# Performance work log

Hardware: AMD Instinct MI355X
Metric: run time of the kernel (lower is better)

The kernel has to match this reference:

```python
import jax, jax.numpy as jnp
import numpy as np

N_QUBITS = 6
N_QPARAMS = 15  # 6*5/2 RBS gates in the pyramid circuit


def _pyramid_top_wires(n):
    """Top wire q of each RBS gate (acting on wires (q, q+1)) in pyramid order.
    Diamond/pyramid layer t has gates at q = |n-2-t|, |n-2-t|+2, ... <= n-2;
    total n(n-1)/2 gates (15 for n=6)."""
    qs = []
    for t in range(2 * n - 3):
        for q in range(abs(n - 2 - t), n - 1, 2):
            qs.append(q)
    return qs


def setup_inputs() -> dict:
    key = jax.random.key(0)
    k0, k1, k2, k3 = jax.random.split(key, 4)
    B, H, W = 16384, 64, 64
    D = H * W  # flattened feature dim
    x = jax.random.normal(k0, (B, H, W, 1), dtype=jnp.float32)
    W1 = jax.random.normal(k1, (D, N_QUBITS), dtype=jnp.float32) / np.float32(np.sqrt(D))
    b1 = jnp.zeros((N_QUBITS,), dtype=jnp.float32)
    # quantum_weights: zeros in the original init; use small randn so grads are non-trivial
    qw = 0.1 * jax.random.normal(k2, (N_QPARAMS,), dtype=jnp.float32)
    W2 = jax.random.normal(k3, (N_QUBITS, 1), dtype=jnp.float32) / np.float32(np.sqrt(N_QUBITS))
    b2 = jnp.zeros((1,), dtype=jnp.float32)
    return {"x": x, "W1": W1, "b1": b1, "qw": qw, "W2": W2, "b2": b2}


def reference(x, W1, b1, qw, W2, b2):
    B = x.shape[0]
    xf = x.reshape(B, -1)                       # Flatten
    h = xf @ W1 + b1                            # Dense(6, linear) -> [B, 6]
    # vector_loader(convert_array(h)): amplitude-encode normalized h in the unary basis
    a = h / jnp.linalg.norm(h, axis=1, keepdims=True)   # [B, 6] unary amplitudes
    # pyramid_circuit: 15 RBS gates == Givens rotations on the 6-dim unary subspace
    for k, q in enumerate(_pyramid_top_wires(N_QUBITS)):
        c, s = jnp.cos(qw[k]), jnp.sin(qw[k])
        aq = c * a[:, q] + s * a[:, q + 1]
        aq1 = -s * a[:, q] + c * a[:, q + 1]
        a = a.at[:, q].set(aq).at[:, q + 1].set(aq1)
    # <Z_i> on unary state sum_i a_i |e_i>  ==  1 - 2 a_i^2
    z = 1.0 - 2.0 * a * a                       # [B, 6]
    z = jnp.where(jnp.isnan(z), jnp.zeros_like(z), z)  # NaN guard from original
    return jax.nn.sigmoid(z @ W2 + b2)          # Dense(1, sigmoid) -> [B, 1]
```

## Files before the change

kernel.cpp:

```cpp
#include <hip/hip_runtime.h>
#include <math.h>

#define DFEAT 4096
#define NQ 6
#define ROWS_PER_WAVE 4
#define WAVES_PER_BLOCK 4
#define ROWS_PER_BLOCK (ROWS_PER_WAVE * WAVES_PER_BLOCK)

__global__ __launch_bounds__(256, 4)
void hybrid_fused_kernel(const float* __restrict__ x,
                         const float* __restrict__ W1,
                         const float* __restrict__ b1,
                         const float* __restrict__ qw,
                         const float* __restrict__ W2,
                         const float* __restrict__ b2,
                         float* __restrict__ out, int B)
{
    const int lane = threadIdx.x & 63;
    const int wave_in_block = threadIdx.x >> 6;
    const int row0 = (blockIdx.x * WAVES_PER_BLOCK + wave_in_block) * ROWS_PER_WAVE;
    if (row0 >= B) return;

    const float* xp[ROWS_PER_WAVE];
#pragma unroll
    for (int r = 0; r < ROWS_PER_WAVE; ++r) {
        int rr = row0 + r; if (rr > B - 1) rr = B - 1;
        xp[r] = x + (size_t)rr * DFEAT;
    }

    float acc[ROWS_PER_WAVE][NQ];
#pragma unroll
    for (int r = 0; r < ROWS_PER_WAVE; ++r)
#pragma unroll
        for (int j = 0; j < NQ; ++j) acc[r][j] = 0.0f;

    for (int it = 0; it < DFEAT / 256; ++it) {
        const int d = it * 256 + lane * 4;

        float w[24];
        const float4* wp = reinterpret_cast<const float4*>(W1 + (size_t)d * NQ);
#pragma unroll
        for (int m = 0; m < 6; ++m)
            reinterpret_cast<float4*>(w)[m] = wp[m];

#pragma unroll
        for (int r = 0; r < ROWS_PER_WAVE; ++r) {
            const float4 xv = *reinterpret_cast<const float4*>(xp[r] + d);
            const float xs[4] = {xv.x, xv.y, xv.z, xv.w};
#pragma unroll
            for (int k = 0; k < 4; ++k)
#pragma unroll
                for (int j = 0; j < NQ; ++j)
                    acc[r][j] = fmaf(xs[k], w[k * NQ + j], acc[r][j]);
        }
    }

#pragma unroll
    for (int r = 0; r < ROWS_PER_WAVE; ++r)
#pragma unroll
        for (int j = 0; j < NQ; ++j) {
            float v = acc[r][j];
#pragma unroll
            for (int off = 32; off >= 1; off >>= 1)
                v += __shfl_xor(v, off, 64);
            acc[r][j] = v;
        }

    if (lane < ROWS_PER_WAVE) {
        float h[NQ];
#pragma unroll
        for (int j = 0; j < NQ; ++j) {
            float v = acc[0][j];
            v = (lane == 1) ? acc[1][j] : v;
            v = (lane == 2) ? acc[2][j] : v;
            v = (lane == 3) ? acc[3][j] : v;
            h[j] = v + b1[j];
        }
        float n2 = 0.0f;
#pragma unroll
        for (int j = 0; j < NQ; ++j) n2 = fmaf(h[j], h[j], n2);
        const float inv = rsqrtf(n2);
        float a[NQ];
#pragma unroll
        for (int j = 0; j < NQ; ++j) a[j] = h[j] * inv;

        const int topw[15] = {4,3,2,4,1,3,0,2,4,1,3,2,4,3,4};
#pragma unroll
        for (int k = 0; k < 15; ++k) {
            const int q = topw[k];
            const float c = cosf(qw[k]);
            const float s = sinf(qw[k]);
            const float aq  = fmaf(c, a[q],     s * a[q + 1]);
            const float aq1 = fmaf(c, a[q + 1], -s * a[q]);
            a[q] = aq;
            a[q + 1] = aq1;
        }

        float zac = b2[0];
#pragma unroll
        for (int j = 0; j < NQ; ++j) {
            float z = 1.0f - 2.0f * a[j] * a[j];
            z = isnan(z) ? 0.0f : z;
            zac = fmaf(z, W2[j], zac);
        }
        const float o = 1.0f / (1.0f + expf(-zac));
        const int row = row0 + lane;
        if (row < B) out[row] = o;
    }
}

extern "C" void kernel_launch(void* const* d_in, const int* in_sizes, int n_in,
                              void* d_out, int out_size, void* d_ws, size_t ws_size,
                              hipStream_t stream) {
    const float* x  = (const float*)d_in[0];
    const float* W1 = (const float*)d_in[1];
    const float* b1 = (const float*)d_in[2];
    const float* qw = (const float*)d_in[3];
    const float* W2 = (const float*)d_in[4];
    const float* b2 = (const float*)d_in[5];
    float* out = (float*)d_out;

    const int B = in_sizes[0] / DFEAT;
    const int blocks = (B + ROWS_PER_BLOCK - 1) / ROWS_PER_BLOCK;
    hybrid_fused_kernel<<<blocks, 256, 0, stream>>>(x, W1, b1, qw, W2, b2, out, B);
}
```

Baseline: 382.6 us.

## Stage W1 slabs through double-buffered LDS transposed, nontemporal x loads

Each block now loads W1 cooperatively into a double-buffered shared-memory slab, transposed to a [feature][d] layout, and prefetches the next slab while computing the current one. Every wave then reads its weights as contiguous vec4 LDS loads instead of each wave separately pulling six float4 values from global memory. The x stream is read with nontemporal loads so it does not evict W1 from cache. The cost is a block-wide barrier every iteration and scattered LDS stores that may hit bank conflicts. The early return for out-of-range rows is removed so that all threads reach the barriers.

```diff
diff --git a/kernel.cpp b/kernel.cpp
--- a/kernel.cpp
+++ b/kernel.cpp
@@ -6,6 +6,11 @@
 #define ROWS_PER_WAVE 4
 #define WAVES_PER_BLOCK 4
 #define ROWS_PER_BLOCK (ROWS_PER_WAVE * WAVES_PER_BLOCK)
+#define SLAB 256
+#define NIT (DFEAT / SLAB)
+#define SLABW (SLAB * NQ)
+
+typedef float floatx4 __attribute__((ext_vector_type(4)));
 
 __global__ __launch_bounds__(256, 4)
 void hybrid_fused_kernel(const float* __restrict__ x,
@@ -16,16 +21,28 @@
                          const float* __restrict__ b2,
                          float* __restrict__ out, int B)
 {
-    const int lane = threadIdx.x & 63;
-    const int wave_in_block = threadIdx.x >> 6;
-    const int row0 = (blockIdx.x * WAVES_PER_BLOCK + wave_in_block) * ROWS_PER_WAVE;
-    if (row0 >= B) return;
+    __shared__ float wl[2][NQ * SLAB];
 
+    const int t = threadIdx.x;
+    const int lane = t & 63;
+    const int wave = t >> 6;
+    int row0 = (blockIdx.x * WAVES_PER_BLOCK + wave) * ROWS_PER_WAVE;
     const float* xp[ROWS_PER_WAVE];
 #pragma unroll
     for (int r = 0; r < ROWS_PER_WAVE; ++r) {
         int rr = row0 + r; if (rr > B - 1) rr = B - 1;
         xp[r] = x + (size_t)rr * DFEAT;
+    }
+
+    int off[6];
+    {
+        const int ws[3] = { 2 * t, 2 * (t + 256), 2 * (t + 512) };
+#pragma unroll
+        for (int p = 0; p < 3; ++p) {
+            const int w = ws[p];
+            off[2 * p]     = (w % NQ) * SLAB + (w / NQ);
+            off[2 * p + 1] = ((w + 1) % NQ) * SLAB + ((w + 1) / NQ);
+        }
     }
 
     float acc[ROWS_PER_WAVE][NQ];
@@ -34,25 +51,55 @@
 #pragma unroll
         for (int j = 0; j < NQ; ++j) acc[r][j] = 0.0f;
 
-    for (int it = 0; it < DFEAT / 256; ++it) {
-        const int d = it * 256 + lane * 4;
+    {
+        const float2* base = reinterpret_cast<const float2*>(W1);
+        const float2 p0 = base[t], p1 = base[t + 256], p2 = base[t + 512];
+        float* wb = wl[0];
+        wb[off[0]] = p0.x; wb[off[1]] = p0.y;
+        wb[off[2]] = p1.x; wb[off[3]] = p1.y;
+        wb[off[4]] = p2.x; wb[off[5]] = p2.y;
+    }
+    __syncthreads();
 
-        float w[24];
-        const float4* wp = reinterpret_cast<const float4*>(W1 + (size_t)d * NQ);
+    for (int it = 0; it < NIT; ++it) {
+        const int cur = it & 1;
+        const int nxt = cur ^ 1;
+
+        float2 q0, q1, q2;
+        const bool pf = (it + 1 < NIT);
+        if (pf) {
+            const float2* base =
+                reinterpret_cast<const float2*>(W1 + (size_t)(it + 1) * SLABW);
+            q0 = base[t]; q1 = base[t + 256]; q2 = base[t + 512];
+        }
+
+        floatx4 wj[NQ];
+        const float* wb = wl[cur];
 #pragma unroll
-        for (int m = 0; m < 6; ++m)
-            reinterpret_cast<float4*>(w)[m] = wp[m];
+        for (int j = 0; j < NQ; ++j)
+            wj[j] = *reinterpret_cast<const floatx4*>(&wb[j * SLAB + lane * 4]);
 
+        const int d = it * SLAB + lane * 4;
 #pragma unroll
         for (int r = 0; r < ROWS_PER_WAVE; ++r) {
-            const float4 xv = *reinterpret_cast<const float4*>(xp[r] + d);
-            const float xs[4] = {xv.x, xv.y, xv.z, xv.w};
+            const floatx4 xv = __builtin_nontemporal_load(
+                reinterpret_cast<const floatx4*>(xp[r] + d));
 #pragma unroll
-            for (int k = 0; k < 4; ++k)
-#pragma unroll
-                for (int j = 0; j < NQ; ++j)
-                    acc[r][j] = fmaf(xs[k], w[k * NQ + j], acc[r][j]);
+            for (int j = 0; j < NQ; ++j) {
+                acc[r][j] = fmaf(xv.x, wj[j].x, acc[r][j]);
+                acc[r][j] = fmaf(xv.y, wj[j].y, acc[r][j]);
+                acc[r][j] = fmaf(xv.z, wj[j].z, acc[r][j]);
+                acc[r][j] = fmaf(xv.w, wj[j].w, acc[r][j]);
+            }
         }
+
+        if (pf) {
+            float* wn = wl[nxt];
+            wn[off[0]] = q0.x; wn[off[1]] = q0.y;
+            wn[off[2]] = q1.x; wn[off[3]] = q1.y;
+            wn[off[4]] = q2.x; wn[off[5]] = q2.y;
+        }
+        __syncthreads();
     }
 
 #pragma unroll
@@ -61,8 +108,8 @@
         for (int j = 0; j < NQ; ++j) {
             float v = acc[r][j];
 #pragma unroll
-            for (int off = 32; off >= 1; off >>= 1)
-                v += __shfl_xor(v, off, 64);
+            for (int offs = 32; offs >= 1; offs >>= 1)
+                v += __shfl_xor(v, offs, 64);
             acc[r][j] = v;
         }
 
```

Measured after the change: 398.1 us. +4.1%, slower.

## Transpose W1 slabs through per-wave LDS and prefetch next x slab

Applied to the files above, without the earlier changes.

Each wave now loads its W1 slab with fully coalesced float2 reads, scatters it into a padded column-major LDS tile, and reads back per-output float4 vectors, replacing the strided 96-byte-per-lane global loads. The x loads for the next slab are issued before the FMAs of the current one, a software pipeline meant to hide global latency. The cost is about 24 KB of shared memory per block, LDS scatter stores with likely bank conflicts, and more registers. No barrier is needed because each wave uses its own LDS region.

```diff
diff --git a/kernel.cpp b/kernel.cpp
--- a/kernel.cpp
+++ b/kernel.cpp
@@ -6,6 +6,12 @@
 #define ROWS_PER_WAVE 4
 #define WAVES_PER_BLOCK 4
 #define ROWS_PER_BLOCK (ROWS_PER_WAVE * WAVES_PER_BLOCK)
+#define SLAB 256
+#define NIT (DFEAT / SLAB)
+#define COLP 257
+
+typedef float floatx4 __attribute__((ext_vector_type(4)));
+typedef float floatx2 __attribute__((ext_vector_type(2)));
 
 __global__ __launch_bounds__(256, 4)
 void hybrid_fused_kernel(const float* __restrict__ x,
@@ -16,9 +22,14 @@
                          const float* __restrict__ b2,
                          float* __restrict__ out, int B)
 {
-    const int lane = threadIdx.x & 63;
-    const int wave_in_block = threadIdx.x >> 6;
-    const int row0 = (blockIdx.x * WAVES_PER_BLOCK + wave_in_block) * ROWS_PER_WAVE;
+    __shared__ float wl_all[WAVES_PER_BLOCK][NQ * COLP];
+
+    const int t = threadIdx.x;
+    const int lane = t & 63;
+    const int wave = t >> 6;
+    float* __restrict__ wl = wl_all[wave];
+
+    const int row0 = (blockIdx.x * WAVES_PER_BLOCK + wave) * ROWS_PER_WAVE;
     if (row0 >= B) return;
 
     const float* xp[ROWS_PER_WAVE];
@@ -28,31 +39,66 @@
         xp[r] = x + (size_t)rr * DFEAT;
     }
 
+    int offe[3], offo[3];
+#pragma unroll
+    for (int p3 = 0; p3 < 3; ++p3) {
+        const int we = 128 * p3 + 2 * lane;
+        const int wo = we + 1;
+        offe[p3] = (we % 6) * COLP + we / 6;
+        offo[p3] = (wo % 6) * COLP + wo / 6;
+    }
+
     float acc[ROWS_PER_WAVE][NQ];
 #pragma unroll
     for (int r = 0; r < ROWS_PER_WAVE; ++r)
 #pragma unroll
         for (int j = 0; j < NQ; ++j) acc[r][j] = 0.0f;
 
-    for (int it = 0; it < DFEAT / 256; ++it) {
-        const int d = it * 256 + lane * 4;
+    floatx4 xv[ROWS_PER_WAVE];
+#pragma unroll
+    for (int r = 0; r < ROWS_PER_WAVE; ++r)
+        xv[r] = *reinterpret_cast<const floatx4*>(xp[r] + lane * 4);
 
-        float w[24];
-        const float4* wp = reinterpret_cast<const float4*>(W1 + (size_t)d * NQ);
+    for (int it = 0; it < NIT; ++it) {
+        floatx2 wv[12];
+        const floatx2* wbase =
+            reinterpret_cast<const floatx2*>(W1 + (size_t)it * SLAB * NQ);
 #pragma unroll
-        for (int m = 0; m < 6; ++m)
-            reinterpret_cast<float4*>(w)[m] = wp[m];
+        for (int p = 0; p < 12; ++p)
+            wv[p] = wbase[p * 64 + lane];
+
+#pragma unroll
+        for (int p = 0; p < 12; ++p) {
+            const int add = 64 * (p / 3);
+            wl[offe[p % 3] + add] = wv[p].x;
+            wl[offo[p % 3] + add] = wv[p].y;
+        }
+
+        floatx4 wj[NQ];
+#pragma unroll
+        for (int j = 0; j < NQ; ++j)
+            wj[j] = *reinterpret_cast<const floatx4*>(&wl[j * COLP + lane * 4]);
+
+        floatx4 xn[ROWS_PER_WAVE];
+        if (it + 1 < NIT) {
+            const int d = (it + 1) * SLAB + lane * 4;
+#pragma unroll
+            for (int r = 0; r < ROWS_PER_WAVE; ++r)
+                xn[r] = *reinterpret_cast<const floatx4*>(xp[r] + d);
+        }
 
 #pragma unroll
         for (int r = 0; r < ROWS_PER_WAVE; ++r) {
-            const float4 xv = *reinterpret_cast<const float4*>(xp[r] + d);
-            const float xs[4] = {xv.x, xv.y, xv.z, xv.w};
 #pragma unroll
-            for (int k = 0; k < 4; ++k)
+            for (int j = 0; j < NQ; ++j) {
+                acc[r][j] = fmaf(xv[r].x, wj[j].x, acc[r][j]);
+                acc[r][j] = fmaf(xv[r].y, wj[j].y, acc[r][j]);
+                acc[r][j] = fmaf(xv[r].z, wj[j].z, acc[r][j]);
+                acc[r][j] = fmaf(xv[r].w, wj[j].w, acc[r][j]);
+            }
+        }
 #pragma unroll
-                for (int j = 0; j < NQ; ++j)
-                    acc[r][j] = fmaf(xs[k], w[k * NQ + j], acc[r][j]);
-        }
+        for (int r = 0; r < ROWS_PER_WAVE; ++r) xv[r] = xn[r];
     }
 
 #pragma unroll
@@ -61,8 +107,8 @@
         for (int j = 0; j < NQ; ++j) {
             float v = acc[r][j];
 #pragma unroll
-            for (int off = 32; off >= 1; off >>= 1)
-                v += __shfl_xor(v, off, 64);
+            for (int offs = 32; offs >= 1; offs >>= 1)
+                v += __shfl_xor(v, offs, 64);
             acc[r][j] = v;
         }
 
```

New measurement: 382.7 us. No clear change (+0.0%).
